# Kernel optimization log

Measured on AMD Instinct MI355X. Metric: run time of the kernel, lower is better.

## Reference

```python
import jax, jax.numpy as jnp
import numpy as np

EMB = 1024
HID = 1024
VOCAB = 50257


def _lstm_cell(x, h, c, Wih, Whh, bih, bhh):
    # PyTorch gate order: i, f, g, o
    gates = x @ Wih.T + bih + h @ Whh.T + bhh  # [1, 4H]
    i, f, g, o = jnp.split(gates, 4, axis=-1)
    c_new = jax.nn.sigmoid(f) * c + jax.nn.sigmoid(i) * jnp.tanh(g)
    h_new = jax.nn.sigmoid(o) * jnp.tanh(c_new)
    return h_new, c_new


def setup_inputs() -> dict:
    key = jax.random.key(0)
    ks = jax.random.split(key, 16)
    s = 0.02
    return {
        "word_input": jax.random.randint(ks[0], (1,), 0, VOCAB),
        "h0": jax.random.normal(ks[1], (2, 1, HID), jnp.float32),
        "c0": jax.random.normal(ks[2], (2, 1, HID), jnp.float32),
        "emb": jax.random.normal(ks[3], (VOCAB, EMB), jnp.float32) * s,
        "W_ih0": jax.random.normal(ks[4], (4 * HID, EMB), jnp.float32) * s,
        "W_hh0": jax.random.normal(ks[5], (4 * HID, HID), jnp.float32) * s,
        "b_ih0": jax.random.normal(ks[6], (4 * HID,), jnp.float32) * s,
        "b_hh0": jax.random.normal(ks[7], (4 * HID,), jnp.float32) * s,
        "W_ih1": jax.random.normal(ks[8], (4 * HID, HID), jnp.float32) * s,
        "W_hh1": jax.random.normal(ks[9], (4 * HID, HID), jnp.float32) * s,
        "b_ih1": jax.random.normal(ks[10], (4 * HID,), jnp.float32) * s,
        "b_hh1": jax.random.normal(ks[11], (4 * HID,), jnp.float32) * s,
        "W_out": jax.random.normal(ks[12], (VOCAB, HID), jnp.float32) * s,
        "b_out": jax.random.normal(ks[13], (VOCAB,), jnp.float32) * s,
    }


def reference(word_input, h0, c0, emb, W_ih0, W_hh0, b_ih0, b_hh0,
              W_ih1, W_hh1, b_ih1, b_hh1, W_out, b_out):
    # embedding lookup + ReLU, batch=1 seq=1
    x = jax.nn.relu(emb[word_input])                 # [1, EMB]
    # 2-layer LSTM single step (dropout disabled / eval mode)
    h1, c1 = _lstm_cell(x, h0[0], c0[0], W_ih0, W_hh0, b_ih0, b_hh0)
    h2, c2 = _lstm_cell(h1, h0[1], c0[1], W_ih1, W_hh1, b_ih1, b_hh1)
    logits = h2 @ W_out.T + b_out                    # [1, VOCAB]
    log_probas = jax.nn.log_softmax(logits, axis=1)
    h_out = jnp.stack([h1, h2])                      # [2, 1, HID]
    c_out = jnp.stack([c1, c2])
    return log_probas, (h_out, c_out)
```

## Files before the change

kernel.cpp:

```cpp
#include <hip/hip_runtime.h>
#include <math.h>

#define EMB 1024
#define HID 1024
#define VOCAB 50257
#define HOUT_OFF VOCAB
#define COUT_OFF (VOCAB + 2*HID)
#define ROWS_PER_BLOCK 16
#define NB_LOGITS ((VOCAB + ROWS_PER_BLOCK - 1) / ROWS_PER_BLOCK)

typedef float f32x4 __attribute__((ext_vector_type(4)));

__device__ __forceinline__ float wave_reduce(float v) {
#pragma unroll
    for (int o = 32; o > 0; o >>= 1) v += __shfl_down(v, o);
    return v;
}

__device__ __forceinline__ float sigmoidf_(float x) { return 1.0f / (1.0f + expf(-x)); }

__global__ __launch_bounds__(256) void lstm_gemv(
    const float* __restrict__ Wih, const float* __restrict__ Whh,
    const float* __restrict__ bih, const float* __restrict__ bhh,
    const float* __restrict__ emb, const int* __restrict__ word,
    const float* __restrict__ x_in,
    const float* __restrict__ h_prev, const float* __restrict__ c_prev,
    float* __restrict__ h_ws, float* __restrict__ out, int layer)
{
    const int r    = blockIdx.x;
    const int wave = threadIdx.x >> 6;
    const int lane = threadIdx.x & 63;
    const int row  = wave * HID + r;

    float4 xv[4], hv[4];
    if (x_in != nullptr) {
#pragma unroll
        for (int j = 0; j < 4; ++j) xv[j] = ((const float4*)x_in)[j*64 + lane];
    } else {
        const float4* e = (const float4*)(emb + (size_t)word[0] * EMB);
#pragma unroll
        for (int j = 0; j < 4; ++j) {
            float4 v = e[j*64 + lane];
            v.x = fmaxf(v.x, 0.f); v.y = fmaxf(v.y, 0.f);
            v.z = fmaxf(v.z, 0.f); v.w = fmaxf(v.w, 0.f);
            xv[j] = v;
        }
    }
#pragma unroll
    for (int j = 0; j < 4; ++j) hv[j] = ((const float4*)h_prev)[j*64 + lane];

    const float4* wih = (const float4*)(Wih + (size_t)row * EMB);
    const float4* whh = (const float4*)(Whh + (size_t)row * HID);
    float acc = 0.f;
#pragma unroll
    for (int j = 0; j < 4; ++j) {
        float4 a = wih[j*64 + lane];
        acc += a.x*xv[j].x + a.y*xv[j].y + a.z*xv[j].z + a.w*xv[j].w;
        float4 b = whh[j*64 + lane];
        acc += b.x*hv[j].x + b.y*hv[j].y + b.z*hv[j].z + b.w*hv[j].w;
    }
    acc = wave_reduce(acc);

    __shared__ float gates[4];
    if (lane == 0) gates[wave] = acc + bih[row] + bhh[row];
    __syncthreads();

    if (threadIdx.x == 0) {
        float ig = sigmoidf_(gates[0]);
        float fg = sigmoidf_(gates[1]);
        float gg = tanhf(gates[2]);
        float og = sigmoidf_(gates[3]);
        float c  = fg * c_prev[r] + ig * gg;
        float h  = og * tanhf(c);
        h_ws[r] = h;
        out[HOUT_OFF + layer * HID + r] = h;
        out[COUT_OFF + layer * HID + r] = c;
    }
}

__global__ __launch_bounds__(256) void logits_gemv(
    const float* __restrict__ W, const float* __restrict__ b,
    const float* __restrict__ x, float* __restrict__ out,
    float* __restrict__ partials)
{
    const int wave = threadIdx.x >> 6;
    const int lane = threadIdx.x & 63;

    f32x4 xv[4];
#pragma unroll
    for (int j = 0; j < 4; ++j) xv[j] = ((const f32x4*)x)[j*64 + lane];

    float m = -INFINITY, s = 0.f;
    const int base = blockIdx.x * ROWS_PER_BLOCK + wave * 4;
#pragma unroll
    for (int k = 0; k < 4; ++k) {
        int row = base + k;
        if (row >= VOCAB) break;
        const f32x4* wr = (const f32x4*)(W + (size_t)row * HID);
        float acc = 0.f;
#pragma unroll
        for (int j = 0; j < 4; ++j) {
            f32x4 a = __builtin_nontemporal_load(wr + j*64 + lane);
            acc += a.x*xv[j].x + a.y*xv[j].y + a.z*xv[j].z + a.w*xv[j].w;
        }
        acc = wave_reduce(acc);
        if (lane == 0) {
            float logit = acc + b[row];
            out[row] = logit;
            float nm = fmaxf(m, logit);
            s = s * expf(m - nm) + expf(logit - nm);
            m = nm;
        }
    }

    __shared__ float ms[4], ss[4];
    if (lane == 0) { ms[wave] = m; ss[wave] = s; }
    __syncthreads();
    if (threadIdx.x == 0) {
        float M = ms[0], S = ss[0];
#pragma unroll
        for (int w = 1; w < 4; ++w) {
            float nm = fmaxf(M, ms[w]);
            S = S * expf(M - nm) + ss[w] * expf(ms[w] - nm);
            M = nm;
        }
        partials[2 * blockIdx.x]     = M;
        partials[2 * blockIdx.x + 1] = S;
    }
}

__global__ __launch_bounds__(256) void lse_sub(
    float* __restrict__ out, const float* __restrict__ partials, int nb)
{
    float M = -INFINITY, S = 0.f;
    for (int p = threadIdx.x; p < nb; p += 256) {
        float m = partials[2*p], s = partials[2*p + 1];
        float nm = fmaxf(M, m);
        S = S * expf(M - nm) + s * expf(m - nm);
        M = nm;
    }
    __shared__ float ms[256], ss[256];
    ms[threadIdx.x] = M; ss[threadIdx.x] = S;
    __syncthreads();
    for (int o = 128; o > 0; o >>= 1) {
        if (threadIdx.x < (unsigned)o) {
            float m2 = ms[threadIdx.x + o], s2 = ss[threadIdx.x + o];
            float m1 = ms[threadIdx.x];
            float nm = fmaxf(m1, m2);
            ss[threadIdx.x] = ss[threadIdx.x] * expf(m1 - nm) + s2 * expf(m2 - nm);
            ms[threadIdx.x] = nm;
        }
        __syncthreads();
    }
    const float lse = ms[0] + logf(ss[0]);

    const int i = blockIdx.x * 256 + (int)threadIdx.x;
    if (i < VOCAB) out[i] -= lse;
}

extern "C" void kernel_launch(void* const* d_in, const int* in_sizes, int n_in,
                              void* d_out, int out_size, void* d_ws, size_t ws_size,
                              hipStream_t stream)
{
    const int*   word = (const int*)  d_in[0];
    const float* h0   = (const float*)d_in[1];
    const float* c0   = (const float*)d_in[2];
    const float* emb  = (const float*)d_in[3];
    const float* Wih0 = (const float*)d_in[4];
    const float* Whh0 = (const float*)d_in[5];
    const float* bih0 = (const float*)d_in[6];
    const float* bhh0 = (const float*)d_in[7];
    const float* Wih1 = (const float*)d_in[8];
    const float* Whh1 = (const float*)d_in[9];
    const float* bih1 = (const float*)d_in[10];
    const float* bhh1 = (const float*)d_in[11];
    const float* Wout = (const float*)d_in[12];
    const float* bout = (const float*)d_in[13];

    float* out = (float*)d_out;
    float* ws  = (float*)d_ws;
    float* h1       = ws;
    float* h2       = ws + HID;
    float* partials = ws + 2 * HID;

    lstm_gemv<<<HID, 256, 0, stream>>>(Wih0, Whh0, bih0, bhh0, emb, word,
                                       nullptr, h0, c0, h1, out, 0);
    lstm_gemv<<<HID, 256, 0, stream>>>(Wih1, Whh1, bih1, bhh1, emb, word,
                                       h1, h0 + HID, c0 + HID, h2, out, 1);
    logits_gemv<<<NB_LOGITS, 256, 0, stream>>>(Wout, bout, h2, out, partials);
    lse_sub<<<(VOCAB + 255) / 256, 256, 0, stream>>>(out, partials, NB_LOGITS);
}
```

Measured before the change: 418.9 us.

## Hoist layer-1 recurrent GEMV into layer-0 kernel to shorten dependency chain

The layer-1 W_hh·h0[1] product does not depend on layer 0, so it now runs in extra blocks of the layer-0 launch and writes partial gate sums plus biases to workspace. The second LSTM kernel then only streams W_ih1 against h1 and adds the precomputed partials. This moves half of layer 1's weight traffic off the serial critical path and lets it share bandwidth with layer 0. LSTM weight loads also switch to nontemporal loads. The cost is an extra workspace round trip for 4*HID partial values.

```diff
diff --git a/kernel.cpp b/kernel.cpp
--- a/kernel.cpp
+++ b/kernel.cpp
@@ -19,50 +19,106 @@
 
 __device__ __forceinline__ float sigmoidf_(float x) { return 1.0f / (1.0f + expf(-x)); }
 
-__global__ __launch_bounds__(256) void lstm_gemv(
-    const float* __restrict__ Wih, const float* __restrict__ Whh,
-    const float* __restrict__ bih, const float* __restrict__ bhh,
-    const float* __restrict__ emb, const int* __restrict__ word,
-    const float* __restrict__ x_in,
-    const float* __restrict__ h_prev, const float* __restrict__ c_prev,
-    float* __restrict__ h_ws, float* __restrict__ out, int layer)
+__global__ __launch_bounds__(256) void lstm0_and_rec1(
+    const float* __restrict__ Wih0, const float* __restrict__ Whh0,
+    const float* __restrict__ bih0, const float* __restrict__ bhh0,
+    const float* __restrict__ Whh1, const float* __restrict__ bih1,
+    const float* __restrict__ bhh1,
+    const float* __restrict__ emb,  const int* __restrict__ word,
+    const float* __restrict__ h0,   const float* __restrict__ c0,
+    float* __restrict__ h1, float* __restrict__ rpart,
+    float* __restrict__ out)
+{
+    const int wave = threadIdx.x >> 6;
+    const int lane = threadIdx.x & 63;
+
+    if (blockIdx.x < HID) {
+        const int r   = blockIdx.x;
+        const int row = wave * HID + r;
+
+        f32x4 xv[4], hv[4];
+        const f32x4* e = (const f32x4*)(emb + (size_t)word[0] * EMB);
+#pragma unroll
+        for (int j = 0; j < 4; ++j) {
+            f32x4 v = e[j*64 + lane];
+            v.x = fmaxf(v.x, 0.f); v.y = fmaxf(v.y, 0.f);
+            v.z = fmaxf(v.z, 0.f); v.w = fmaxf(v.w, 0.f);
+            xv[j] = v;
+            hv[j] = ((const f32x4*)h0)[j*64 + lane];
+        }
+
+        const f32x4* wih = (const f32x4*)(Wih0 + (size_t)row * EMB);
+        const f32x4* whh = (const f32x4*)(Whh0 + (size_t)row * HID);
+        float acc = 0.f;
+#pragma unroll
+        for (int j = 0; j < 4; ++j) {
+            f32x4 a = __builtin_nontemporal_load(wih + j*64 + lane);
+            acc += a.x*xv[j].x + a.y*xv[j].y + a.z*xv[j].z + a.w*xv[j].w;
+            f32x4 b = __builtin_nontemporal_load(whh + j*64 + lane);
+            acc += b.x*hv[j].x + b.y*hv[j].y + b.z*hv[j].z + b.w*hv[j].w;
+        }
+        acc = wave_reduce(acc);
+
+        __shared__ float gates[4];
+        if (lane == 0) gates[wave] = acc + bih0[row] + bhh0[row];
+        __syncthreads();
+
+        if (threadIdx.x == 0) {
+            float ig = sigmoidf_(gates[0]);
+            float fg = sigmoidf_(gates[1]);
+            float gg = tanhf(gates[2]);
+            float og = sigmoidf_(gates[3]);
+            float c  = fg * c0[r] + ig * gg;
+            float h  = og * tanhf(c);
+            h1[r] = h;
+            out[HOUT_OFF + r] = h;
+            out[COUT_OFF + r] = c;
+        }
+    } else {
+        const int r   = blockIdx.x - HID;
+        const int row = wave * HID + r;
+
+        f32x4 hv[4];
+#pragma unroll
+        for (int j = 0; j < 4; ++j) hv[j] = ((const f32x4*)(h0 + HID))[j*64 + lane];
+
+        const f32x4* whh = (const f32x4*)(Whh1 + (size_t)row * HID);
+        float acc = 0.f;
+#pragma unroll
+        for (int j = 0; j < 4; ++j) {
+            f32x4 b = __builtin_nontemporal_load(whh + j*64 + lane);
+            acc += b.x*hv[j].x + b.y*hv[j].y + b.z*hv[j].z + b.w*hv[j].w;
+        }
+        acc = wave_reduce(acc);
+        if (lane == 0) rpart[row] = acc + bih1[row] + bhh1[row];
+    }
+}
+
+__global__ __launch_bounds__(256) void lstm1_gemv(
+    const float* __restrict__ Wih1, const float* __restrict__ h1,
+    const float* __restrict__ rpart, const float* __restrict__ c_prev,
+    float* __restrict__ h2, float* __restrict__ out)
 {
     const int r    = blockIdx.x;
     const int wave = threadIdx.x >> 6;
     const int lane = threadIdx.x & 63;
     const int row  = wave * HID + r;
 
-    float4 xv[4], hv[4];
-    if (x_in != nullptr) {
-#pragma unroll
-        for (int j = 0; j < 4; ++j) xv[j] = ((const float4*)x_in)[j*64 + lane];
-    } else {
-        const float4* e = (const float4*)(emb + (size_t)word[0] * EMB);
-#pragma unroll
-        for (int j = 0; j < 4; ++j) {
-            float4 v = e[j*64 + lane];
-            v.x = fmaxf(v.x, 0.f); v.y = fmaxf(v.y, 0.f);
-            v.z = fmaxf(v.z, 0.f); v.w = fmaxf(v.w, 0.f);
-            xv[j] = v;
-        }
-    }
-#pragma unroll
-    for (int j = 0; j < 4; ++j) hv[j] = ((const float4*)h_prev)[j*64 + lane];
-
-    const float4* wih = (const float4*)(Wih + (size_t)row * EMB);
-    const float4* whh = (const float4*)(Whh + (size_t)row * HID);
+    f32x4 xv[4];
+#pragma unroll
+    for (int j = 0; j < 4; ++j) xv[j] = ((const f32x4*)h1)[j*64 + lane];
+
+    const f32x4* wih = (const f32x4*)(Wih1 + (size_t)row * HID);
     float acc = 0.f;
 #pragma unroll
     for (int j = 0; j < 4; ++j) {
-        float4 a = wih[j*64 + lane];
+        f32x4 a = __builtin_nontemporal_load(wih + j*64 + lane);
         acc += a.x*xv[j].x + a.y*xv[j].y + a.z*xv[j].z + a.w*xv[j].w;
-        float4 b = whh[j*64 + lane];
-        acc += b.x*hv[j].x + b.y*hv[j].y + b.z*hv[j].z + b.w*hv[j].w;
     }
     acc = wave_reduce(acc);
 
     __shared__ float gates[4];
-    if (lane == 0) gates[wave] = acc + bih[row] + bhh[row];
+    if (lane == 0) gates[wave] = acc + rpart[row];
     __syncthreads();
 
     if (threadIdx.x == 0) {
@@ -72,9 +128,9 @@
         float og = sigmoidf_(gates[3]);
         float c  = fg * c_prev[r] + ig * gg;
         float h  = og * tanhf(c);
-        h_ws[r] = h;
-        out[HOUT_OFF + layer * HID + r] = h;
-        out[COUT_OFF + layer * HID + r] = c;
+        h2[r] = h;
+        out[HOUT_OFF + HID + r] = h;
+        out[COUT_OFF + HID + r] = c;
     }
 }
 
@@ -181,12 +237,13 @@
     float* ws  = (float*)d_ws;
     float* h1       = ws;
     float* h2       = ws + HID;
-    float* partials = ws + 2 * HID;
-
-    lstm_gemv<<<HID, 256, 0, stream>>>(Wih0, Whh0, bih0, bhh0, emb, word,
-                                       nullptr, h0, c0, h1, out, 0);
-    lstm_gemv<<<HID, 256, 0, stream>>>(Wih1, Whh1, bih1, bhh1, emb, word,
-                                       h1, h0 + HID, c0 + HID, h2, out, 1);
+    float* rpart    = ws + 2 * HID;
+    float* partials = ws + 6 * HID;
+
+    lstm0_and_rec1<<<2 * HID, 256, 0, stream>>>(
+        Wih0, Whh0, bih0, bhh0, Whh1, bih1, bhh1,
+        emb, word, h0, c0, h1, rpart, out);
+    lstm1_gemv<<<HID, 256, 0, stream>>>(Wih1, h1, rpart, c0 + HID, h2, out);
     logits_gemv<<<NB_LOGITS, 256, 0, stream>>>(Wout, bout, h2, out, partials);
     lse_sub<<<(VOCAB + 255) / 256, 256, 0, stream>>>(out, partials, NB_LOGITS);
 }
```

Result: no change. 412.4 us (-1.5%).
